# Kernel optimization log

Hardware: AMD Instinct MI355X
Metric: run time of the kernel (lower is better)

Reference implementation:

```python
import jax, jax.numpy as jnp
import numpy as np

C = 256
CQ = C // 8
B, H, W = 4, 64, 64


def setup_inputs() -> dict:
    key = jax.random.key(0)
    ks = jax.random.split(key, 8)
    x = jax.random.normal(ks[0], (B, C, H, W), dtype=jnp.float32)
    # 1x1 conv weights stored as [out, in]
    wq = jax.random.normal(ks[1], (CQ, C), dtype=jnp.float32) * 0.02
    bq = jnp.zeros((CQ,), dtype=jnp.float32)
    wk = jax.random.normal(ks[2], (CQ, C), dtype=jnp.float32) * 0.02
    bk = jnp.zeros((CQ,), dtype=jnp.float32)
    wv = jax.random.normal(ks[3], (C, C), dtype=jnp.float32) * 0.02
    bv = jnp.zeros((C,), dtype=jnp.float32)
    # gamma initialized nonzero so output depends on attention path
    gamma = jnp.ones((1,), dtype=jnp.float32) * 0.5
    return {"x": x, "wq": wq, "bq": bq, "wk": wk, "bk": bk,
            "wv": wv, "bv": bv, "gamma": gamma}


def reference(x, wq, bq, wk, bk, wv, bv, gamma):
    Bx, Cx, Hx, Wx = x.shape
    N = Hx * Wx
    xf = x.reshape(Bx, Cx, N)                      # [B, C, N]
    q = jnp.einsum('oc,bcn->bon', wq, xf) + bq[None, :, None]  # [B, C/8, N]
    k = jnp.einsum('oc,bcn->bon', wk, xf) + bk[None, :, None]  # [B, C/8, N]
    v = jnp.einsum('oc,bcn->bon', wv, xf) + bv[None, :, None]  # [B, C, N]
    # attn[b,i,j] = softmax_j( sum_d q[b,d,i] * k[b,d,j] )  (no scale factor)
    scores = jnp.einsum('bdi,bdj->bij', q, k)      # [B, N, N]
    attn = jax.nn.softmax(scores, axis=-1)
    # out[b,c,i] = sum_j v[b,c,j] * attn[b,i,j]
    out = jnp.einsum('bcj,bij->bci', v, attn).reshape(Bx, Cx, Hx, Wx)
    return gamma[0] * out + x
```

## Files before the change

kernel.cpp:

```cpp
#include <hip/hip_runtime.h>
#include <math.h>

#define NPIX 4096
#define CH   256
#define CQD  32
#define LOG2E 1.44269504088896340736f

typedef float f32x4 __attribute__((ext_vector_type(4)));
typedef short s16x8 __attribute__((ext_vector_type(8)));

__device__ __forceinline__ unsigned short f2bf(float f) {
  unsigned u = __builtin_bit_cast(unsigned, f);
  return (unsigned short)((u + 0x7FFFu + ((u >> 16) & 1u)) >> 16);
}

__device__ __forceinline__ f32x4 mfma16(s16x8 a, s16x8 b, f32x4 c) {
  return __builtin_amdgcn_mfma_f32_16x16x32_bf16(a, b, c, 0, 0, 0);
}

__device__ __forceinline__ float fexp2(float x) {
#if __has_builtin(__builtin_amdgcn_exp2f)
  return __builtin_amdgcn_exp2f(x);
#else
  return exp2f(x);
#endif
}

__device__ __forceinline__ float frcp(float x) {
#if __has_builtin(__builtin_amdgcn_rcpf)
  return __builtin_amdgcn_rcpf(x);
#else
  return 1.0f / x;
#endif
}

__global__ __launch_bounds__(256) void wpack_kernel(
    const float* __restrict__ wq, const float* __restrict__ wk,
    const float* __restrict__ wv, unsigned short* __restrict__ Wp)
{
  const int row = blockIdx.x;
  const int c = threadIdx.x;
  float v;
  if (row < 32)      v = wq[row * CH + c] * LOG2E;
  else if (row < 64) v = wk[(row - 32) * CH + c];
  else               v = wv[(row - 64) * CH + c];
  Wp[(size_t)row * CH + c] = f2bf(v);
}

__global__ __launch_bounds__(256) void proj_kernel(
    const float* __restrict__ x, const unsigned short* __restrict__ Wp,
    const float* __restrict__ bq, const float* __restrict__ bk,
    const float* __restrict__ bv,
    unsigned short* __restrict__ Qb, unsigned short* __restrict__ Kb,
    unsigned short* __restrict__ Vb)
{
  __shared__ unsigned short Xs[64][264];

  const int blk = blockIdx.x;
  const int tile = blk & 255;
  const int split = blk >> 8;
  const int b  = tile >> 6;
  const int i0 = (tile & 63) * 64;
  const int tid = threadIdx.x;
  const int w = tid >> 6;
  const int lane = tid & 63;
  const int g = lane >> 4;
  const int r = lane & 15;

  {
    const int i  = tid & 63;
    const int cs = (tid >> 6) * 4;
    const float* xb = x + (size_t)b * CH * NPIX + i0 + i;
    #pragma unroll
    for (int cc = cs; cc < CH; cc += 16) {
      float f0 = xb[(size_t)(cc + 0) * NPIX];
      float f1 = xb[(size_t)(cc + 1) * NPIX];
      float f2 = xb[(size_t)(cc + 2) * NPIX];
      float f3 = xb[(size_t)(cc + 3) * NPIX];
      ushort4 pk;
      pk.x = f2bf(f0); pk.y = f2bf(f1); pk.z = f2bf(f2); pk.w = f2bf(f3);
      *(ushort4*)&Xs[i][cc] = pk;
    }
  }
  __syncthreads();

  const int dt = split * 4 + w;
  const unsigned short* wrow = Wp + (size_t)(dt * 16 + r) * CH;

  f32x4 acc[4];
  #pragma unroll
  for (int is = 0; is < 4; ++is) { acc[is][0]=0.f; acc[is][1]=0.f; acc[is][2]=0.f; acc[is][3]=0.f; }

  #pragma unroll
  for (int kt = 0; kt < 8; ++kt) {
    const s16x8 af = *(const s16x8*)&wrow[kt * 32 + g * 8];
    #pragma unroll
    for (int is = 0; is < 4; ++is) {
      const s16x8 bf = *(const s16x8*)&Xs[is * 16 + r][kt * 32 + g * 8];
      acc[is] = mfma16(af, bf, acc[is]);
    }
  }

  if (dt < 4) {
    const int dloc = (dt & 1) * 16;
    const float* bp = (dt < 2) ? bq : bk;
    float4 bias = *(const float4*)&bp[dloc + g * 4];
    if (dt < 2) { bias.x *= LOG2E; bias.y *= LOG2E; bias.z *= LOG2E; bias.w *= LOG2E; }
    unsigned short* dst = (dt < 2) ? Qb : Kb;
    #pragma unroll
    for (int is = 0; is < 4; ++is) {
      const int i = i0 + is * 16 + r;
      ushort4 pk;
      pk.x = f2bf(acc[is][0] + bias.x);
      pk.y = f2bf(acc[is][1] + bias.y);
      pk.z = f2bf(acc[is][2] + bias.z);
      pk.w = f2bf(acc[is][3] + bias.w);
      *(ushort4*)&dst[((size_t)b * NPIX + i) * CQD + dloc + g * 4] = pk;
    }
  } else {
    const int dloc = (dt - 4) * 16;
    const float4 bias = *(const float4*)&bv[dloc + g * 4];
    #pragma unroll
    for (int is = 0; is < 4; ++is) {
      const int i = i0 + is * 16 + r;
      Vb[((size_t)b * CH + dloc + g * 4 + 0) * NPIX + i] = f2bf(acc[is][0] + bias.x);
      Vb[((size_t)b * CH + dloc + g * 4 + 1) * NPIX + i] = f2bf(acc[is][1] + bias.y);
      Vb[((size_t)b * CH + dloc + g * 4 + 2) * NPIX + i] = f2bf(acc[is][2] + bias.z);
      Vb[((size_t)b * CH + dloc + g * 4 + 3) * NPIX + i] = f2bf(acc[is][3] + bias.w);
    }
  }
}

__global__ __launch_bounds__(256, 2) void attn_kernel(
    const unsigned short* __restrict__ Qb, const unsigned short* __restrict__ Kb,
    const unsigned short* __restrict__ Vb, const float* __restrict__ x,
    const float* __restrict__ gamma, float* __restrict__ out)
{
  __shared__ __align__(16) unsigned char smem[4 * 64 * 33 * 4];
  __shared__ float l_s[64];

  typedef unsigned short PsArr[64][88];
  PsArr* Ps = (PsArr*)smem;

  const int blk = blockIdx.x;
  const int xcd = blk & 7;
  const int b = xcd >> 1;
  const int split = xcd & 1;
  const int i0 = (blk >> 3) * 64;

  const int tid = threadIdx.x;
  const int w = tid >> 6;
  const int lane = tid & 63;
  const int g = lane >> 4;
  const int r = lane & 15;
  const int c0 = split * 128 + w * 32;

  const unsigned short* __restrict__ Qbase = Qb + (size_t)b * NPIX * CQD;
  const unsigned short* __restrict__ Kbase = Kb + (size_t)b * NPIX * CQD;
  const unsigned short* __restrict__ Vbase = Vb + (size_t)b * CH * NPIX;

  const s16x8 qf = *(const s16x8*)&Qbase[(size_t)(i0 + w * 16 + r) * CQD + g * 8];

  s16x8 ones;
  #pragma unroll
  for (int j = 0; j < 8; ++j) ones[j] = (short)0x3F80;

  f32x4 o[4][2];
  f32x4 o_l[4];
  #pragma unroll
  for (int is = 0; is < 4; ++is) {
    o_l[is][0]=0.f; o_l[is][1]=0.f; o_l[is][2]=0.f; o_l[is][3]=0.f;
    #pragma unroll
    for (int ct = 0; ct < 2; ++ct) { o[is][ct][0]=0.f; o[is][ct][1]=0.f; o[is][ct][2]=0.f; o[is][ct][3]=0.f; }
  }

  s16x8 kf0 = *(const s16x8*)&Kbase[(size_t)( 0 + r) * CQD + g * 8];
  s16x8 kf1 = *(const s16x8*)&Kbase[(size_t)(16 + r) * CQD + g * 8];
  s16x8 kf2 = *(const s16x8*)&Kbase[(size_t)(32 + r) * CQD + g * 8];
  s16x8 kf3 = *(const s16x8*)&Kbase[(size_t)(48 + r) * CQD + g * 8];
  const unsigned short* vpa = Vbase + (size_t)(c0 +      r) * NPIX + g * 8;
  const unsigned short* vpb = Vbase + (size_t)(c0 + 16 + r) * NPIX + g * 8;
  s16x8 vfa0 = *(const s16x8*)vpa;
  s16x8 vfa1 = *(const s16x8*)(vpa + 32);
  s16x8 vfb0 = *(const s16x8*)vpb;
  s16x8 vfb1 = *(const s16x8*)(vpb + 32);

  #pragma unroll 1
  for (int t = 0; t < 64; ++t) {
    const int cur = t & 1;
    const f32x4 z = {0.f, 0.f, 0.f, 0.f};
    f32x4 s0 = mfma16(qf, kf0, z);
    f32x4 s1 = mfma16(qf, kf1, z);
    f32x4 s2 = mfma16(qf, kf2, z);
    f32x4 s3 = mfma16(qf, kf3, z);

    const int jn = ((t + 1) & 63) * 64;
    const s16x8 nkf0 = *(const s16x8*)&Kbase[(size_t)(jn +  0 + r) * CQD + g * 8];
    const s16x8 nkf1 = *(const s16x8*)&Kbase[(size_t)(jn + 16 + r) * CQD + g * 8];
    const s16x8 nkf2 = *(const s16x8*)&Kbase[(size_t)(jn + 32 + r) * CQD + g * 8];
    const s16x8 nkf3 = *(const s16x8*)&Kbase[(size_t)(jn + 48 + r) * CQD + g * 8];
    const unsigned short* nvpa = Vbase + (size_t)(c0 +      r) * NPIX + jn + g * 8;
    const unsigned short* nvpb = Vbase + (size_t)(c0 + 16 + r) * NPIX + jn + g * 8;
    const s16x8 nvfa0 = *(const s16x8*)nvpa;
    const s16x8 nvfa1 = *(const s16x8*)(nvpa + 32);
    const s16x8 nvfb0 = *(const s16x8*)nvpb;
    const s16x8 nvfb1 = *(const s16x8*)(nvpb + 32);

    #pragma unroll
    for (int e = 0; e < 4; ++e) {
      const int row = w * 16 + g * 4 + e;
      Ps[cur][row][ 0 + r] = f2bf(fexp2(s0[e]));
      Ps[cur][row][16 + r] = f2bf(fexp2(s1[e]));
      Ps[cur][row][32 + r] = f2bf(fexp2(s2[e]));
      Ps[cur][row][48 + r] = f2bf(fexp2(s3[e]));
    }

    __syncthreads();

    #pragma unroll
    for (int is = 0; is < 4; ++is) {
      const s16x8 pf0 = *(const s16x8*)&Ps[cur][is * 16 + r][ 0 + g * 8];
      const s16x8 pf1 = *(const s16x8*)&Ps[cur][is * 16 + r][32 + g * 8];
      o[is][0] = mfma16(pf0, vfa0, o[is][0]);
      o[is][0] = mfma16(pf1, vfa1, o[is][0]);
      o[is][1] = mfma16(pf0, vfb0, o[is][1]);
      o[is][1] = mfma16(pf1, vfb1, o[is][1]);
      if (w == 3) {
        o_l[is] = mfma16(pf0, ones, o_l[is]);
        o_l[is] = mfma16(pf1, ones, o_l[is]);
      }
    }

    kf0 = nkf0; kf1 = nkf1; kf2 = nkf2; kf3 = nkf3;
    vfa0 = nvfa0; vfa1 = nvfa1; vfb0 = nvfb0; vfb1 = nvfb1;
  }

  if (w == 3 && r == 0) {
    #pragma unroll
    for (int is = 0; is < 4; ++is)
      #pragma unroll
      for (int e = 0; e < 4; ++e)
        l_s[is * 16 + g * 4 + e] = o_l[is][e];
  }
  __syncthreads();

  float* otp = ((float*)smem) + (size_t)w * (64 * 33);
  #pragma unroll
  for (int is = 0; is < 4; ++is) {
    #pragma unroll
    for (int e = 0; e < 4; ++e) {
      const int row = is * 16 + g * 4 + e;
      const float rl = frcp(l_s[row]);
      otp[row * 33 +      r] = o[is][0][e] * rl;
      otp[row * 33 + 16 + r] = o[is][1][e] * rl;
    }
  }

  const float gam = gamma[0];
  const size_t obase = ((size_t)b * CH + c0) * NPIX + i0 + lane;
  #pragma unroll 1
  for (int cl = 0; cl < 32; ++cl) {
    const size_t off = obase + (size_t)cl * NPIX;
    out[off] = gam * otp[lane * 33 + cl] + x[off];
  }
}

extern "C" void kernel_launch(void* const* d_in, const int* in_sizes, int n_in,
                              void* d_out, int out_size, void* d_ws, size_t ws_size,
                              hipStream_t stream) {
  const float* x     = (const float*)d_in[0];
  const float* wq    = (const float*)d_in[1];
  const float* bq    = (const float*)d_in[2];
  const float* wk    = (const float*)d_in[3];
  const float* bk    = (const float*)d_in[4];
  const float* wv    = (const float*)d_in[5];
  const float* bv    = (const float*)d_in[6];
  const float* gamma = (const float*)d_in[7];
  float* out = (float*)d_out;

  unsigned short* Qb = (unsigned short*)d_ws;
  unsigned short* Kb = Qb + (size_t)4 * NPIX * CQD;
  unsigned short* Vb = Kb + (size_t)4 * NPIX * CQD;
  unsigned short* Wp = Vb + (size_t)4 * CH * NPIX;

  hipLaunchKernelGGL(wpack_kernel, dim3(320), dim3(256), 0, stream, wq, wk, wv, Wp);
  hipLaunchKernelGGL(proj_kernel, dim3(1280), dim3(256), 0, stream,
                     x, Wp, bq, bk, bv, Qb, Kb, Vb);
  hipLaunchKernelGGL(attn_kernel, dim3(512), dim3(256), 0, stream,
                     Qb, Kb, Vb, x, gamma, out);
}
```

Before: 190.3 us.

## Split x transpose into separate kernel, restructure projection, double attention grid

Adds an xt_kernel that transposes x into a pixel-major bf16 buffer, so the projection kernel can load its MFMA operands straight from global memory without an LDS staging step. The projection kernel is reorganised so each block handles 16 pixels across all 320 output rows; V is now written with vectorised ushort4 stores. The attention kernel splits channels four ways instead of two, giving 1024 blocks of 16 channels per wave, with a smaller LDS footprint and a launch-bounds occupancy hint of 4. The cost is an extra kernel launch and a round trip of the transposed x through memory. In attention, each block now recomputes QK^T and the exponentials for only half as many channels, doubling that redundant work.

Result: slower. 233.5 us (+22.7%).

```diff
diff --git a/kernel.cpp b/kernel.cpp
--- a/kernel.cpp
+++ b/kernel.cpp
@@ -47,96 +47,129 @@
   Wp[(size_t)row * CH + c] = f2bf(v);
 }
 
-__global__ __launch_bounds__(256) void proj_kernel(
-    const float* __restrict__ x, const unsigned short* __restrict__ Wp,
+__global__ __launch_bounds__(256) void xt_kernel(
+    const float* __restrict__ x, unsigned short* __restrict__ Xt)
+{
+  __shared__ float Lf[64][65];
+
+  const int blk = blockIdx.x;
+  const int pt = blk & 63;
+  const int ct = (blk >> 6) & 3;
+  const int b  = blk >> 8;
+  const int t = threadIdx.x;
+
+  {
+    const int px4 = (t & 15) * 4;
+    const int cl  = t >> 4;
+    const float* xb = x + ((size_t)b * CH + ct * 64) * NPIX + (size_t)pt * 64;
+    #pragma unroll
+    for (int it = 0; it < 4; ++it) {
+      const int c = cl + it * 16;
+      const float4 v = *(const float4*)&xb[(size_t)c * NPIX + px4];
+      Lf[c][px4 + 0] = v.x;
+      Lf[c][px4 + 1] = v.y;
+      Lf[c][px4 + 2] = v.z;
+      Lf[c][px4 + 3] = v.w;
+    }
+  }
+  __syncthreads();
+
+  {
+    const int c4 = (t & 15) * 4;
+    const int pl = t >> 4;
+    unsigned short* xtb = Xt + ((size_t)b * NPIX + (size_t)pt * 64) * CH + ct * 64;
+    #pragma unroll
+    for (int it = 0; it < 4; ++it) {
+      const int px = pl + it * 16;
+      ushort4 pk;
+      pk.x = f2bf(Lf[c4 + 0][px]);
+      pk.y = f2bf(Lf[c4 + 1][px]);
+      pk.z = f2bf(Lf[c4 + 2][px]);
+      pk.w = f2bf(Lf[c4 + 3][px]);
+      *(ushort4*)&xtb[(size_t)px * CH + c4] = pk;
+    }
+  }
+}
+
+__global__ __launch_bounds__(256, 4) void proj_kernel(
+    const unsigned short* __restrict__ Xt, const unsigned short* __restrict__ Wp,
     const float* __restrict__ bq, const float* __restrict__ bk,
     const float* __restrict__ bv,
     unsigned short* __restrict__ Qb, unsigned short* __restrict__ Kb,
     unsigned short* __restrict__ Vb)
 {
-  __shared__ unsigned short Xs[64][264];
-
   const int blk = blockIdx.x;
-  const int tile = blk & 255;
-  const int split = blk >> 8;
-  const int b  = tile >> 6;
-  const int i0 = (tile & 63) * 64;
+  const int pt = blk & 255;
+  const int b  = blk >> 8;
   const int tid = threadIdx.x;
   const int w = tid >> 6;
   const int lane = tid & 63;
   const int g = lane >> 4;
   const int r = lane & 15;
 
+  const unsigned short* xtp = Xt + ((size_t)b * NPIX + pt * 16 + r) * CH + g * 8;
+  s16x8 xf[8];
+  #pragma unroll
+  for (int kt = 0; kt < 8; ++kt) xf[kt] = *(const s16x8*)&xtp[kt * 32];
+
+  f32x4 acc[5];
+  #pragma unroll
+  for (int dd = 0; dd < 5; ++dd) { acc[dd][0]=0.f; acc[dd][1]=0.f; acc[dd][2]=0.f; acc[dd][3]=0.f; }
+
+  #pragma unroll
+  for (int dd = 0; dd < 5; ++dd) {
+    const int dt = dd * 4 + w;
+    const unsigned short* wp = Wp + (size_t)(dt * 16 + r) * CH + g * 8;
+    if (dd == 0) {
+      #pragma unroll
+      for (int kt = 0; kt < 8; ++kt) {
+        const s16x8 wf = *(const s16x8*)&wp[kt * 32];
+        acc[0] = mfma16(wf, xf[kt], acc[0]);
+      }
+    } else {
+      #pragma unroll
+      for (int kt = 0; kt < 8; ++kt) {
+        const s16x8 wf = *(const s16x8*)&wp[kt * 32];
+        acc[dd] = mfma16(xf[kt], wf, acc[dd]);
+      }
+    }
+  }
+
   {
-    const int i  = tid & 63;
-    const int cs = (tid >> 6) * 4;
-    const float* xb = x + (size_t)b * CH * NPIX + i0 + i;
-    #pragma unroll
-    for (int cc = cs; cc < CH; cc += 16) {
-      float f0 = xb[(size_t)(cc + 0) * NPIX];
-      float f1 = xb[(size_t)(cc + 1) * NPIX];
-      float f2 = xb[(size_t)(cc + 2) * NPIX];
-      float f3 = xb[(size_t)(cc + 3) * NPIX];
-      ushort4 pk;
-      pk.x = f2bf(f0); pk.y = f2bf(f1); pk.z = f2bf(f2); pk.w = f2bf(f3);
-      *(ushort4*)&Xs[i][cc] = pk;
-    }
-  }
-  __syncthreads();
-
-  const int dt = split * 4 + w;
-  const unsigned short* wrow = Wp + (size_t)(dt * 16 + r) * CH;
-
-  f32x4 acc[4];
-  #pragma unroll
-  for (int is = 0; is < 4; ++is) { acc[is][0]=0.f; acc[is][1]=0.f; acc[is][2]=0.f; acc[is][3]=0.f; }
-
-  #pragma unroll
-  for (int kt = 0; kt < 8; ++kt) {
-    const s16x8 af = *(const s16x8*)&wrow[kt * 32 + g * 8];
-    #pragma unroll
-    for (int is = 0; is < 4; ++is) {
-      const s16x8 bf = *(const s16x8*)&Xs[is * 16 + r][kt * 32 + g * 8];
-      acc[is] = mfma16(af, bf, acc[is]);
-    }
-  }
-
-  if (dt < 4) {
+    const int dt = w;
     const int dloc = (dt & 1) * 16;
     const float* bp = (dt < 2) ? bq : bk;
     float4 bias = *(const float4*)&bp[dloc + g * 4];
     if (dt < 2) { bias.x *= LOG2E; bias.y *= LOG2E; bias.z *= LOG2E; bias.w *= LOG2E; }
     unsigned short* dst = (dt < 2) ? Qb : Kb;
-    #pragma unroll
-    for (int is = 0; is < 4; ++is) {
-      const int i = i0 + is * 16 + r;
-      ushort4 pk;
-      pk.x = f2bf(acc[is][0] + bias.x);
-      pk.y = f2bf(acc[is][1] + bias.y);
-      pk.z = f2bf(acc[is][2] + bias.z);
-      pk.w = f2bf(acc[is][3] + bias.w);
-      *(ushort4*)&dst[((size_t)b * NPIX + i) * CQD + dloc + g * 4] = pk;
-    }
-  } else {
-    const int dloc = (dt - 4) * 16;
-    const float4 bias = *(const float4*)&bv[dloc + g * 4];
-    #pragma unroll
-    for (int is = 0; is < 4; ++is) {
-      const int i = i0 + is * 16 + r;
-      Vb[((size_t)b * CH + dloc + g * 4 + 0) * NPIX + i] = f2bf(acc[is][0] + bias.x);
-      Vb[((size_t)b * CH + dloc + g * 4 + 1) * NPIX + i] = f2bf(acc[is][1] + bias.y);
-      Vb[((size_t)b * CH + dloc + g * 4 + 2) * NPIX + i] = f2bf(acc[is][2] + bias.z);
-      Vb[((size_t)b * CH + dloc + g * 4 + 3) * NPIX + i] = f2bf(acc[is][3] + bias.w);
-    }
-  }
-}
-
-__global__ __launch_bounds__(256, 2) void attn_kernel(
+    ushort4 pk;
+    pk.x = f2bf(acc[0][0] + bias.x);
+    pk.y = f2bf(acc[0][1] + bias.y);
+    pk.z = f2bf(acc[0][2] + bias.z);
+    pk.w = f2bf(acc[0][3] + bias.w);
+    *(ushort4*)&dst[((size_t)b * NPIX + pt * 16 + r) * CQD + dloc + g * 4] = pk;
+  }
+
+  #pragma unroll
+  for (int dd = 1; dd < 5; ++dd) {
+    const int dt = dd * 4 + w;
+    const int vch = (dt - 4) * 16 + r;
+    const float bias = bv[vch];
+    ushort4 pk;
+    pk.x = f2bf(acc[dd][0] + bias);
+    pk.y = f2bf(acc[dd][1] + bias);
+    pk.z = f2bf(acc[dd][2] + bias);
+    pk.w = f2bf(acc[dd][3] + bias);
+    *(ushort4*)&Vb[((size_t)b * CH + vch) * NPIX + pt * 16 + g * 4] = pk;
+  }
+}
+
+__global__ __launch_bounds__(256, 4) void attn_kernel(
     const unsigned short* __restrict__ Qb, const unsigned short* __restrict__ Kb,
     const unsigned short* __restrict__ Vb, const float* __restrict__ x,
     const float* __restrict__ gamma, float* __restrict__ out)
 {
-  __shared__ __align__(16) unsigned char smem[4 * 64 * 33 * 4];
+  __shared__ __align__(16) unsigned char smem[2 * 64 * 88 * 2];
   __shared__ float l_s[64];
 
   typedef unsigned short PsArr[64][88];
@@ -145,15 +178,15 @@
   const int blk = blockIdx.x;
   const int xcd = blk & 7;
   const int b = xcd >> 1;
-  const int split = xcd & 1;
-  const int i0 = (blk >> 3) * 64;
+  const int split = ((blk >> 3) & 1) * 2 + (xcd & 1);
+  const int i0 = (blk >> 4) * 64;
 
   const int tid = threadIdx.x;
   const int w = tid >> 6;
   const int lane = tid & 63;
   const int g = lane >> 4;
   const int r = lane & 15;
-  const int c0 = split * 128 + w * 32;
+  const int c0 = split * 64 + w * 16;
 
   const unsigned short* __restrict__ Qbase = Qb + (size_t)b * NPIX * CQD;
   const unsigned short* __restrict__ Kbase = Kb + (size_t)b * NPIX * CQD;
@@ -165,25 +198,21 @@
   #pragma unroll
   for (int j = 0; j < 8; ++j) ones[j] = (short)0x3F80;
 
-  f32x4 o[4][2];
+  f32x4 o[4];
   f32x4 o_l[4];
   #pragma unroll
   for (int is = 0; is < 4; ++is) {
+    o[is][0]=0.f; o[is][1]=0.f; o[is][2]=0.f; o[is][3]=0.f;
     o_l[is][0]=0.f; o_l[is][1]=0.f; o_l[is][2]=0.f; o_l[is][3]=0.f;
-    #pragma unroll
-    for (int ct = 0; ct < 2; ++ct) { o[is][ct][0]=0.f; o[is][ct][1]=0.f; o[is][ct][2]=0.f; o[is][ct][3]=0.f; }
   }
 
   s16x8 kf0 = *(const s16x8*)&Kbase[(size_t)( 0 + r) * CQD + g * 8];
   s16x8 kf1 = *(const s16x8*)&Kbase[(size_t)(16 + r) * CQD + g * 8];
   s16x8 kf2 = *(const s16x8*)&Kbase[(size_t)(32 + r) * CQD + g * 8];
   s16x8 kf3 = *(const s16x8*)&Kbase[(size_t)(48 + r) * CQD + g * 8];
-  const unsigned short* vpa = Vbase + (size_t)(c0 +      r) * NPIX + g * 8;
-  const unsigned short* vpb = Vbase + (size_t)(c0 + 16 + r) * NPIX + g * 8;
-  s16x8 vfa0 = *(const s16x8*)vpa;
-  s16x8 vfa1 = *(const s16x8*)(vpa + 32);
-  s16x8 vfb0 = *(const s16x8*)vpb;
-  s16x8 vfb1 = *(const s16x8*)(vpb + 32);
+  const unsigned short* vp = Vbase + (size_t)(c0 + r) * NPIX + g * 8;
+  s16x8 vf0 = *(const s16x8*)vp;
+  s16x8 vf1 = *(const s16x8*)(vp + 32);
 
   #pragma unroll 1
   for (int t = 0; t < 64; ++t) {
@@ -199,12 +228,9 @@
     const s16x8 nkf1 = *(const s16x8*)&Kbase[(size_t)(jn + 16 + r) * CQD + g * 8];
     const s16x8 nkf2 = *(const s16x8*)&Kbase[(size_t)(jn + 32 + r) * CQD + g * 8];
     const s16x8 nkf3 = *(const s16x8*)&Kbase[(size_t)(jn + 48 + r) * CQD + g * 8];
-    const unsigned short* nvpa = Vbase + (size_t)(c0 +      r) * NPIX + jn + g * 8;
-    const unsigned short* nvpb = Vbase + (size_t)(c0 + 16 + r) * NPIX + jn + g * 8;
-    const s16x8 nvfa0 = *(const s16x8*)nvpa;
-    const s16x8 nvfa1 = *(const s16x8*)(nvpa + 32);
-    const s16x8 nvfb0 = *(const s16x8*)nvpb;
-    const s16x8 nvfb1 = *(const s16x8*)(nvpb + 32);
+    const unsigned short* nvp = Vbase + (size_t)(c0 + r) * NPIX + jn + g * 8;
+    const s16x8 nvf0 = *(const s16x8*)nvp;
+    const s16x8 nvf1 = *(const s16x8*)(nvp + 32);
 
     #pragma unroll
     for (int e = 0; e < 4; ++e) {
@@ -221,10 +247,8 @@
     for (int is = 0; is < 4; ++is) {
       const s16x8 pf0 = *(const s16x8*)&Ps[cur][is * 16 + r][ 0 + g * 8];
       const s16x8 pf1 = *(const s16x8*)&Ps[cur][is * 16 + r][32 + g * 8];
-      o[is][0] = mfma16(pf0, vfa0, o[is][0]);
-      o[is][0] = mfma16(pf1, vfa1, o[is][0]);
-      o[is][1] = mfma16(pf0, vfb0, o[is][1]);
-      o[is][1] = mfma16(pf1, vfb1, o[is][1]);
+      o[is] = mfma16(pf0, vf0, o[is]);
+      o[is] = mfma16(pf1, vf1, o[is]);
       if (w == 3) {
         o_l[is] = mfma16(pf0, ones, o_l[is]);
         o_l[is] = mfma16(pf1, ones, o_l[is]);
@@ -232,7 +256,7 @@
     }
 
     kf0 = nkf0; kf1 = nkf1; kf2 = nkf2; kf3 = nkf3;
-    vfa0 = nvfa0; vfa1 = nvfa1; vfb0 = nvfb0; vfb1 = nvfb1;
+    vf0 = nvf0; vf1 = nvf1;
   }
 
   if (w == 3 && r == 0) {
@@ -244,24 +268,22 @@
   }
   __syncthreads();
 
-  float* otp = ((float*)smem) + (size_t)w * (64 * 33);
+  float* otp = ((float*)smem) + (size_t)w * (64 * 17);
   #pragma unroll
   for (int is = 0; is < 4; ++is) {
     #pragma unroll
     for (int e = 0; e < 4; ++e) {
       const int row = is * 16 + g * 4 + e;
-      const float rl = frcp(l_s[row]);
-      otp[row * 33 +      r] = o[is][0][e] * rl;
-      otp[row * 33 + 16 + r] = o[is][1][e] * rl;
+      otp[row * 17 + r] = o[is][e] * frcp(l_s[row]);
     }
   }
 
   const float gam = gamma[0];
   const size_t obase = ((size_t)b * CH + c0) * NPIX + i0 + lane;
   #pragma unroll 1
-  for (int cl = 0; cl < 32; ++cl) {
+  for (int cl = 0; cl < 16; ++cl) {
     const size_t off = obase + (size_t)cl * NPIX;
-    out[off] = gam * otp[lane * 33 + cl] + x[off];
+    out[off] = gam * otp[lane * 17 + cl] + x[off];
   }
 }
 
@@ -282,10 +304,12 @@
   unsigned short* Kb = Qb + (size_t)4 * NPIX * CQD;
   unsigned short* Vb = Kb + (size_t)4 * NPIX * CQD;
   unsigned short* Wp = Vb + (size_t)4 * CH * NPIX;
+  unsigned short* Xt = Wp + (size_t)320 * CH;
 
   hipLaunchKernelGGL(wpack_kernel, dim3(320), dim3(256), 0, stream, wq, wk, wv, Wp);
-  hipLaunchKernelGGL(proj_kernel, dim3(1280), dim3(256), 0, stream,
-                     x, Wp, bq, bk, bv, Qb, Kb, Vb);
-  hipLaunchKernelGGL(attn_kernel, dim3(512), dim3(256), 0, stream,
+  hipLaunchKernelGGL(xt_kernel,   dim3(1024), dim3(256), 0, stream, x, Xt);
+  hipLaunchKernelGGL(proj_kernel, dim3(1024), dim3(256), 0, stream,
+                     Xt, Wp, bq, bk, bv, Qb, Kb, Vb);
+  hipLaunchKernelGGL(attn_kernel, dim3(1024), dim3(256), 0, stream,
                      Qb, Kb, Vb, x, gamma, out);
 }
```

## Restructure projection and attention kernels with transposed MFMA and packed bf16 conversion

Applied to the files above, without the earlier changes.

The projection kernel now uses 512-thread blocks that each compute all 320 output rows for one 64-pixel tile. This removes the 5x redundant reload and conversion of x across split blocks. The attention kernel swaps MFMA operand order so each wave computes one K tile against all four Q tiles, writes P with packed v_cvt_pk_bf16 stores, and writes outputs directly from registers instead of staging them through shared memory. The risks are higher register pressure, lower occupancy in the projection kernel, and less coalesced output stores.

Result: faster. 165.8 us (-12.9%).

```diff
diff --git a/kernel.cpp b/kernel.cpp
--- a/kernel.cpp
+++ b/kernel.cpp
@@ -12,6 +12,12 @@
 __device__ __forceinline__ unsigned short f2bf(float f) {
   unsigned u = __builtin_bit_cast(unsigned, f);
   return (unsigned short)((u + 0x7FFFu + ((u >> 16) & 1u)) >> 16);
+}
+
+__device__ __forceinline__ unsigned cvt_pk_bf16(float a, float b) {
+  unsigned d;
+  asm("v_cvt_pk_bf16_f32 %0, %1, %2" : "=v"(d) : "v"(a), "v"(b));
+  return d;
 }
 
 __device__ __forceinline__ f32x4 mfma16(s16x8 a, s16x8 b, f32x4 c) {
@@ -47,7 +53,7 @@
   Wp[(size_t)row * CH + c] = f2bf(v);
 }
 
-__global__ __launch_bounds__(256) void proj_kernel(
+__global__ __launch_bounds__(512, 2) void proj_kernel(
     const float* __restrict__ x, const unsigned short* __restrict__ Wp,
     const float* __restrict__ bq, const float* __restrict__ bk,
     const float* __restrict__ bv,
@@ -57,76 +63,88 @@
   __shared__ unsigned short Xs[64][264];
 
   const int blk = blockIdx.x;
-  const int tile = blk & 255;
-  const int split = blk >> 8;
-  const int b  = tile >> 6;
-  const int i0 = (tile & 63) * 64;
-  const int tid = threadIdx.x;
-  const int w = tid >> 6;
-  const int lane = tid & 63;
+  const int b  = blk >> 6;
+  const int p0 = (blk & 63) * 64;
+  const int t = threadIdx.x;
+  const int w = t >> 6;
+  const int lane = t & 63;
   const int g = lane >> 4;
   const int r = lane & 15;
 
   {
-    const int i  = tid & 63;
-    const int cs = (tid >> 6) * 4;
-    const float* xb = x + (size_t)b * CH * NPIX + i0 + i;
-    #pragma unroll
-    for (int cc = cs; cc < CH; cc += 16) {
-      float f0 = xb[(size_t)(cc + 0) * NPIX];
-      float f1 = xb[(size_t)(cc + 1) * NPIX];
-      float f2 = xb[(size_t)(cc + 2) * NPIX];
-      float f3 = xb[(size_t)(cc + 3) * NPIX];
-      ushort4 pk;
-      pk.x = f2bf(f0); pk.y = f2bf(f1); pk.z = f2bf(f2); pk.w = f2bf(f3);
-      *(ushort4*)&Xs[i][cc] = pk;
+    const int px = t & 63;
+    const int cb = (t >> 6) * 4;
+    const float* xb = x + (size_t)b * CH * NPIX + p0 + px;
+    #pragma unroll
+    for (int it = 0; it < 8; ++it) {
+      const int c = cb + it * 32;
+      const float f0 = xb[(size_t)(c + 0) * NPIX];
+      const float f1 = xb[(size_t)(c + 1) * NPIX];
+      const float f2 = xb[(size_t)(c + 2) * NPIX];
+      const float f3 = xb[(size_t)(c + 3) * NPIX];
+      uint2 pk;
+      pk.x = cvt_pk_bf16(f0, f1);
+      pk.y = cvt_pk_bf16(f2, f3);
+      *(uint2*)&Xs[px][c] = pk;
     }
   }
   __syncthreads();
 
-  const int dt = split * 4 + w;
-  const unsigned short* wrow = Wp + (size_t)(dt * 16 + r) * CH;
-
-  f32x4 acc[4];
-  #pragma unroll
-  for (int is = 0; is < 4; ++is) { acc[is][0]=0.f; acc[is][1]=0.f; acc[is][2]=0.f; acc[is][3]=0.f; }
+  const int ndd = (w < 4) ? 3 : 2;
+
+  f32x4 acc[3][4];
+  #pragma unroll
+  for (int dd = 0; dd < 3; ++dd)
+    #pragma unroll
+    for (int ps = 0; ps < 4; ++ps) { acc[dd][ps][0]=0.f; acc[dd][ps][1]=0.f; acc[dd][ps][2]=0.f; acc[dd][ps][3]=0.f; }
 
   #pragma unroll
   for (int kt = 0; kt < 8; ++kt) {
-    const s16x8 af = *(const s16x8*)&wrow[kt * 32 + g * 8];
-    #pragma unroll
-    for (int is = 0; is < 4; ++is) {
-      const s16x8 bf = *(const s16x8*)&Xs[is * 16 + r][kt * 32 + g * 8];
-      acc[is] = mfma16(af, bf, acc[is]);
-    }
-  }
-
-  if (dt < 4) {
-    const int dloc = (dt & 1) * 16;
-    const float* bp = (dt < 2) ? bq : bk;
-    float4 bias = *(const float4*)&bp[dloc + g * 4];
-    if (dt < 2) { bias.x *= LOG2E; bias.y *= LOG2E; bias.z *= LOG2E; bias.w *= LOG2E; }
-    unsigned short* dst = (dt < 2) ? Qb : Kb;
-    #pragma unroll
-    for (int is = 0; is < 4; ++is) {
-      const int i = i0 + is * 16 + r;
-      ushort4 pk;
-      pk.x = f2bf(acc[is][0] + bias.x);
-      pk.y = f2bf(acc[is][1] + bias.y);
-      pk.z = f2bf(acc[is][2] + bias.z);
-      pk.w = f2bf(acc[is][3] + bias.w);
-      *(ushort4*)&dst[((size_t)b * NPIX + i) * CQD + dloc + g * 4] = pk;
-    }
-  } else {
-    const int dloc = (dt - 4) * 16;
-    const float4 bias = *(const float4*)&bv[dloc + g * 4];
-    #pragma unroll
-    for (int is = 0; is < 4; ++is) {
-      const int i = i0 + is * 16 + r;
-      Vb[((size_t)b * CH + dloc + g * 4 + 0) * NPIX + i] = f2bf(acc[is][0] + bias.x);
-      Vb[((size_t)b * CH + dloc + g * 4 + 1) * NPIX + i] = f2bf(acc[is][1] + bias.y);
-      Vb[((size_t)b * CH + dloc + g * 4 + 2) * NPIX + i] = f2bf(acc[is][2] + bias.z);
-      Vb[((size_t)b * CH + dloc + g * 4 + 3) * NPIX + i] = f2bf(acc[is][3] + bias.w);
+    s16x8 xf[4];
+    #pragma unroll
+    for (int ps = 0; ps < 4; ++ps)
+      xf[ps] = *(const s16x8*)&Xs[ps * 16 + r][kt * 32 + g * 8];
+    #pragma unroll
+    for (int dd = 0; dd < 3; ++dd) {
+      if (dd >= ndd) continue;
+      const int dt = w + dd * 8;
+      const s16x8 wf = *(const s16x8*)&Wp[(size_t)(dt * 16 + r) * CH + kt * 32 + g * 8];
+      if (dt < 4) {
+        #pragma unroll
+        for (int ps = 0; ps < 4; ++ps) acc[dd][ps] = mfma16(xf[ps], wf, acc[dd][ps]);
+      } else {
+        #pragma unroll
+        for (int ps = 0; ps < 4; ++ps) acc[dd][ps] = mfma16(wf, xf[ps], acc[dd][ps]);
+      }
+    }
+  }
+
+  #pragma unroll
+  for (int dd = 0; dd < 3; ++dd) {
+    if (dd >= ndd) continue;
+    const int dt = w + dd * 8;
+    if (dt < 4) {
+      const int dloc = (dt & 1) * 16;
+      float bias = (dt < 2) ? bq[dloc + r] * LOG2E : bk[dloc + r];
+      unsigned short* dst = (dt < 2) ? Qb : Kb;
+      #pragma unroll
+      for (int ps = 0; ps < 4; ++ps)
+        #pragma unroll
+        for (int e = 0; e < 4; ++e) {
+          const int px = p0 + ps * 16 + 4 * g + e;
+          dst[((size_t)b * NPIX + px) * CQD + dloc + r] = f2bf(acc[dd][ps][e] + bias);
+        }
+    } else {
+      const int c0v = (dt - 4) * 16;
+      const float4 b4 = *(const float4*)&bv[c0v + 4 * g];
+      #pragma unroll
+      for (int ps = 0; ps < 4; ++ps) {
+        const int px = p0 + ps * 16 + r;
+        Vb[((size_t)b * CH + c0v + 4 * g + 0) * NPIX + px] = f2bf(acc[dd][ps][0] + b4.x);
+        Vb[((size_t)b * CH + c0v + 4 * g + 1) * NPIX + px] = f2bf(acc[dd][ps][1] + b4.y);
+        Vb[((size_t)b * CH + c0v + 4 * g + 2) * NPIX + px] = f2bf(acc[dd][ps][2] + b4.z);
+        Vb[((size_t)b * CH + c0v + 4 * g + 3) * NPIX + px] = f2bf(acc[dd][ps][3] + b4.w);
+      }
     }
   }
 }
@@ -136,11 +154,8 @@
     const unsigned short* __restrict__ Vb, const float* __restrict__ x,
     const float* __restrict__ gamma, float* __restrict__ out)
 {
-  __shared__ __align__(16) unsigned char smem[4 * 64 * 33 * 4];
+  __shared__ __align__(16) unsigned short Ps[2][64][72];
   __shared__ float l_s[64];
-
-  typedef unsigned short PsArr[64][88];
-  PsArr* Ps = (PsArr*)smem;
 
   const int blk = blockIdx.x;
   const int xcd = blk & 7;
@@ -159,110 +174,101 @@
   const unsigned short* __restrict__ Kbase = Kb + (size_t)b * NPIX * CQD;
   const unsigned short* __restrict__ Vbase = Vb + (size_t)b * CH * NPIX;
 
-  const s16x8 qf = *(const s16x8*)&Qbase[(size_t)(i0 + w * 16 + r) * CQD + g * 8];
+  s16x8 qf[4];
+  #pragma unroll
+  for (int is = 0; is < 4; ++is)
+    qf[is] = *(const s16x8*)&Qbase[(size_t)(i0 + is * 16 + r) * CQD + g * 8];
 
   s16x8 ones;
   #pragma unroll
   for (int j = 0; j < 8; ++j) ones[j] = (short)0x3F80;
 
   f32x4 o[4][2];
-  f32x4 o_l[4];
-  #pragma unroll
-  for (int is = 0; is < 4; ++is) {
-    o_l[is][0]=0.f; o_l[is][1]=0.f; o_l[is][2]=0.f; o_l[is][3]=0.f;
-    #pragma unroll
-    for (int ct = 0; ct < 2; ++ct) { o[is][ct][0]=0.f; o[is][ct][1]=0.f; o[is][ct][2]=0.f; o[is][ct][3]=0.f; }
-  }
-
-  s16x8 kf0 = *(const s16x8*)&Kbase[(size_t)( 0 + r) * CQD + g * 8];
-  s16x8 kf1 = *(const s16x8*)&Kbase[(size_t)(16 + r) * CQD + g * 8];
-  s16x8 kf2 = *(const s16x8*)&Kbase[(size_t)(32 + r) * CQD + g * 8];
-  s16x8 kf3 = *(const s16x8*)&Kbase[(size_t)(48 + r) * CQD + g * 8];
-  const unsigned short* vpa = Vbase + (size_t)(c0 +      r) * NPIX + g * 8;
-  const unsigned short* vpb = Vbase + (size_t)(c0 + 16 + r) * NPIX + g * 8;
-  s16x8 vfa0 = *(const s16x8*)vpa;
-  s16x8 vfa1 = *(const s16x8*)(vpa + 32);
-  s16x8 vfb0 = *(const s16x8*)vpb;
-  s16x8 vfb1 = *(const s16x8*)(vpb + 32);
-
-  #pragma unroll 1
+  f32x4 o_l = {0.f, 0.f, 0.f, 0.f};
+  #pragma unroll
+  for (int is = 0; is < 4; ++is)
+    #pragma unroll
+    for (int cs = 0; cs < 2; ++cs) { o[is][cs][0]=0.f; o[is][cs][1]=0.f; o[is][cs][2]=0.f; o[is][cs][3]=0.f; }
+
+  s16x8 kf = *(const s16x8*)&Kbase[(size_t)(w * 16 + r) * CQD + g * 8];
+  s16x8 vf[2][2];
+  #pragma unroll
+  for (int cs = 0; cs < 2; ++cs)
+    #pragma unroll
+    for (int ks = 0; ks < 2; ++ks)
+      vf[cs][ks] = *(const s16x8*)&Vbase[(size_t)(c0 + cs * 16 + r) * NPIX + ks * 32 + g * 8];
+
+  #pragma unroll 2
   for (int t = 0; t < 64; ++t) {
     const int cur = t & 1;
     const f32x4 z = {0.f, 0.f, 0.f, 0.f};
-    f32x4 s0 = mfma16(qf, kf0, z);
-    f32x4 s1 = mfma16(qf, kf1, z);
-    f32x4 s2 = mfma16(qf, kf2, z);
-    f32x4 s3 = mfma16(qf, kf3, z);
+
+    f32x4 s[4];
+    #pragma unroll
+    for (int is = 0; is < 4; ++is) s[is] = mfma16(kf, qf[is], z);
 
     const int jn = ((t + 1) & 63) * 64;
-    const s16x8 nkf0 = *(const s16x8*)&Kbase[(size_t)(jn +  0 + r) * CQD + g * 8];
-    const s16x8 nkf1 = *(const s16x8*)&Kbase[(size_t)(jn + 16 + r) * CQD + g * 8];
-    const s16x8 nkf2 = *(const s16x8*)&Kbase[(size_t)(jn + 32 + r) * CQD + g * 8];
-    const s16x8 nkf3 = *(const s16x8*)&Kbase[(size_t)(jn + 48 + r) * CQD + g * 8];
-    const unsigned short* nvpa = Vbase + (size_t)(c0 +      r) * NPIX + jn + g * 8;
-    const unsigned short* nvpb = Vbase + (size_t)(c0 + 16 + r) * NPIX + jn + g * 8;
-    const s16x8 nvfa0 = *(const s16x8*)nvpa;
-    const s16x8 nvfa1 = *(const s16x8*)(nvpa + 32);
-    const s16x8 nvfb0 = *(const s16x8*)nvpb;
-    const s16x8 nvfb1 = *(const s16x8*)(nvpb + 32);
-
-    #pragma unroll
-    for (int e = 0; e < 4; ++e) {
-      const int row = w * 16 + g * 4 + e;
-      Ps[cur][row][ 0 + r] = f2bf(fexp2(s0[e]));
-      Ps[cur][row][16 + r] = f2bf(fexp2(s1[e]));
-      Ps[cur][row][32 + r] = f2bf(fexp2(s2[e]));
-      Ps[cur][row][48 + r] = f2bf(fexp2(s3[e]));
+    const s16x8 nkf = *(const s16x8*)&Kbase[(size_t)(jn + w * 16 + r) * CQD + g * 8];
+    s16x8 nvf[2][2];
+    #pragma unroll
+    for (int cs = 0; cs < 2; ++cs)
+      #pragma unroll
+      for (int ks = 0; ks < 2; ++ks)
+        nvf[cs][ks] = *(const s16x8*)&Vbase[(size_t)(c0 + cs * 16 + r) * NPIX + jn + ks * 32 + g * 8];
+
+    #pragma unroll
+    for (int is = 0; is < 4; ++is) {
+      const float p0v = fexp2(s[is][0]);
+      const float p1v = fexp2(s[is][1]);
+      const float p2v = fexp2(s[is][2]);
+      const float p3v = fexp2(s[is][3]);
+      uint2 pk;
+      pk.x = cvt_pk_bf16(p0v, p1v);
+      pk.y = cvt_pk_bf16(p2v, p3v);
+      *(uint2*)&Ps[cur][is * 16 + r][w * 16 + 4 * g] = pk;
     }
 
     __syncthreads();
 
     #pragma unroll
     for (int is = 0; is < 4; ++is) {
-      const s16x8 pf0 = *(const s16x8*)&Ps[cur][is * 16 + r][ 0 + g * 8];
-      const s16x8 pf1 = *(const s16x8*)&Ps[cur][is * 16 + r][32 + g * 8];
-      o[is][0] = mfma16(pf0, vfa0, o[is][0]);
-      o[is][0] = mfma16(pf1, vfa1, o[is][0]);
-      o[is][1] = mfma16(pf0, vfb0, o[is][1]);
-      o[is][1] = mfma16(pf1, vfb1, o[is][1]);
-      if (w == 3) {
-        o_l[is] = mfma16(pf0, ones, o_l[is]);
-        o_l[is] = mfma16(pf1, ones, o_l[is]);
-      }
-    }
-
-    kf0 = nkf0; kf1 = nkf1; kf2 = nkf2; kf3 = nkf3;
-    vfa0 = nvfa0; vfa1 = nvfa1; vfb0 = nvfb0; vfb1 = nvfb1;
-  }
-
-  if (w == 3 && r == 0) {
-    #pragma unroll
-    for (int is = 0; is < 4; ++is)
-      #pragma unroll
-      for (int e = 0; e < 4; ++e)
-        l_s[is * 16 + g * 4 + e] = o_l[is][e];
-  }
+      const s16x8 pb0 = *(const s16x8*)&Ps[cur][is * 16 + r][g * 8];
+      const s16x8 pb1 = *(const s16x8*)&Ps[cur][is * 16 + r][32 + g * 8];
+      o[is][0] = mfma16(vf[0][0], pb0, o[is][0]);
+      o[is][0] = mfma16(vf[0][1], pb1, o[is][0]);
+      o[is][1] = mfma16(vf[1][0], pb0, o[is][1]);
+      o[is][1] = mfma16(vf[1][1], pb1, o[is][1]);
+      if (is == w) {
+        o_l = mfma16(ones, pb0, o_l);
+        o_l = mfma16(ones, pb1, o_l);
+      }
+    }
+
+    kf = nkf;
+    #pragma unroll
+    for (int cs = 0; cs < 2; ++cs)
+      #pragma unroll
+      for (int ks = 0; ks < 2; ++ks) vf[cs][ks] = nvf[cs][ks];
+  }
+
+  if (g == 0) l_s[w * 16 + r] = o_l[0];
   __syncthreads();
 
-  float* otp = ((float*)smem) + (size_t)w * (64 * 33);
-  #pragma unroll
-  for (int is = 0; is < 4; ++is) {
-    #pragma unroll
-    for (int e = 0; e < 4; ++e) {
-      const int row = is * 16 + g * 4 + e;
-      const float rl = frcp(l_s[row]);
-      otp[row * 33 +      r] = o[is][0][e] * rl;
-      otp[row * 33 + 16 + r] = o[is][1][e] * rl;
-    }
-  }
+  float rl[4];
+  #pragma unroll
+  for (int is = 0; is < 4; ++is) rl[is] = frcp(l_s[is * 16 + r]);
 
   const float gam = gamma[0];
-  const size_t obase = ((size_t)b * CH + c0) * NPIX + i0 + lane;
-  #pragma unroll 1
-  for (int cl = 0; cl < 32; ++cl) {
-    const size_t off = obase + (size_t)cl * NPIX;
-    out[off] = gam * otp[lane * 33 + cl] + x[off];
-  }
+  #pragma unroll
+  for (int is = 0; is < 4; ++is)
+    #pragma unroll
+    for (int cs = 0; cs < 2; ++cs)
+      #pragma unroll
+      for (int e = 0; e < 4; ++e) {
+        const int ch = c0 + cs * 16 + 4 * g + e;
+        const size_t off = ((size_t)b * CH + ch) * NPIX + i0 + is * 16 + r;
+        out[off] = gam * o[is][cs][e] * rl[is] + x[off];
+      }
 }
 
 extern "C" void kernel_launch(void* const* d_in, const int* in_sizes, int n_in,
@@ -284,8 +290,8 @@
   unsigned short* Wp = Vb + (size_t)4 * CH * NPIX;
 
   hipLaunchKernelGGL(wpack_kernel, dim3(320), dim3(256), 0, stream, wq, wk, wv, Wp);
-  hipLaunchKernelGGL(proj_kernel, dim3(1280), dim3(256), 0, stream,
+  hipLaunchKernelGGL(proj_kernel,  dim3(256), dim3(512), 0, stream,
                      x, Wp, bq, bk, bv, Qb, Kb, Vb);
-  hipLaunchKernelGGL(attn_kernel, dim3(512), dim3(256), 0, stream,
+  hipLaunchKernelGGL(attn_kernel,  dim3(512), dim3(256), 0, stream,
                      Qb, Kb, Vb, x, gamma, out);
 }
```
